# Optimization experiments

Hardware: AMD Instinct MI355X
Metric: run time of the kernel (lower is better)

## Reference

```python
import jax, jax.numpy as jnp
import numpy as np

DIMS = [128, 118, 109, 100, 92]  # dims[i+1] = max(int(dims[i]/1.081), 6)
NUM_SHELLS = 3
TARGET_COORD = 1.081
NUM_BASINS = 8
BATCH = 12288


def _pdist(a, b):
    # Euclidean pairwise distances [Na, Nb]
    a2 = jnp.sum(a * a, axis=-1)
    b2 = jnp.sum(b * b, axis=-1)
    d2 = a2[:, None] + b2[None, :] - 2.0 * (a @ b.T)
    return jnp.sqrt(jnp.clip(d2, 0.0, None))


def setup_inputs() -> dict:
    key = jax.random.key(0)
    ks = jax.random.split(key, 32)
    inp = {"x": jax.random.normal(ks[0], (BATCH, DIMS[0]), jnp.float32)}
    i = 1
    for s in range(4):
        din, dout = DIMS[s], DIMS[s + 1]
        sc = 1.0 / np.sqrt(din)
        inp[f"cw{s}"] = jax.random.uniform(ks[i], (dout, din), jnp.float32, -sc, sc); i += 1
        inp[f"cb{s}"] = jax.random.uniform(ks[i], (dout,), jnp.float32, -sc, sc); i += 1
        sc0 = 1.0 / np.sqrt(DIMS[0])
        inp[f"sw{s}"] = jax.random.uniform(ks[i], (dout, DIMS[0]), jnp.float32, -sc0, sc0); i += 1
        inp[f"sb{s}"] = jax.random.uniform(ks[i], (dout,), jnp.float32, -sc0, sc0); i += 1
    D = DIMS[-1]
    inp["shell_bnd"] = jnp.linspace(0.5, 2.0, NUM_SHELLS + 1, dtype=jnp.float32)
    scs = 1.0 / np.sqrt(NUM_SHELLS)
    inp["se_w"] = jax.random.uniform(ks[i], (D, NUM_SHELLS), jnp.float32, -scs, scs); i += 1
    inp["se_b"] = jax.random.uniform(ks[i], (D,), jnp.float32, -scs, scs); i += 1
    inp["basin_c"] = jax.random.normal(ks[i], (NUM_BASINS, D), jnp.float32) * 0.1; i += 1
    inp["basin_d"] = jnp.linspace(-6.48, -7.68, NUM_BASINS, dtype=jnp.float32)
    inp["basin_w"] = jnp.ones((NUM_BASINS,), jnp.float32) * 0.5
    return inp


def _forward(x, cws, cbs, sws, sbs, shell_bnd, se_w, se_b, basin_c, basin_d, basin_w):
    # CompressionTransform: Linear -> GELU (+ 0.1 * skip from input)
    cur = x
    for w, b, w2, b2 in zip(cws, cbs, sws, sbs):
        cur = jax.nn.gelu(cur @ w.T + b, approximate=False) + 0.1 * (x @ w2.T + b2)
    compressed = cur  # [B, 92]

    # EnergyLandscape: softmax basin mixture
    bdists = _pdist(compressed, basin_c)             # [B, num_basins]
    widths = jax.nn.softplus(basin_w)                # [num_basins]
    basin_probs = jax.nn.softmax(-bdists / widths, axis=-1)
    energy = jnp.sum(basin_probs * basin_d, axis=-1)  # [B]

    # CoordinationAnalysis: pairwise-distance shell histogram
    B = compressed.shape[0]
    dself = _pdist(compressed, compressed)           # [B, B]
    offdiag = ~jnp.eye(B, dtype=bool)
    bnd = jax.nn.softplus(shell_bnd)
    occ = jnp.stack(
        [jnp.sum(jnp.where(offdiag & (dself >= bnd[i]) & (dself < bnd[i + 1]), 1.0, 0.0), axis=-1)
         for i in range(NUM_SHELLS)],
        axis=-1,
    )  # [B, num_shells]
    occ = occ / (TARGET_COORD * (B - 1) + 1e-08)
    feats = compressed + occ @ se_w.T + se_b          # features with coordination info
    return feats, energy, basin_probs, occ


def reference(x, cw0, cb0, sw0, sb0, cw1, cb1, sw1, sb1, cw2, cb2, sw2, sb2,
              cw3, cb3, sw3, sb3, shell_bnd, se_w, se_b, basin_c, basin_d, basin_w):
    cws = [cw0, cw1, cw2, cw3]
    cbs = [cb0, cb1, cb2, cb3]
    sws = [sw0, sw1, sw2, sw3]
    sbs = [sb0, sb1, sb2, sb3]
    return _forward(x, cws, cbs, sws, sbs, shell_bnd, se_w, se_b, basin_c, basin_d, basin_w)
```

## Files before the change

kernel.cpp:

```cpp
#include <hip/hip_runtime.h>
#include <hip/hip_bf16.h>

typedef __attribute__((ext_vector_type(8))) short bf16x8;
typedef __attribute__((ext_vector_type(4))) float f32x4;
typedef unsigned short u16;

#define BATCH 12288

__device__ __forceinline__ u16 f2bf(float f){
  __hip_bfloat16 h = __float2bfloat16(f);
  return *reinterpret_cast<u16*>(&h);
}
__device__ __forceinline__ float bf2f(u16 u){
  __hip_bfloat16 h; *reinterpret_cast<u16*>(&h) = u;
  return __bfloat162float(h);
}
__device__ __forceinline__ f32x4 mfma16(bf16x8 a, bf16x8 b, f32x4 c){
  return __builtin_amdgcn_mfma_f32_16x16x32_bf16(a, b, c, 0, 0, 0);
}
__device__ __forceinline__ float softplusf(float v){ return log1pf(expf(v)); }

__global__ __launch_bounds__(256) void k_wconv8(
    const float* __restrict__ s0, const float* __restrict__ s1,
    const float* __restrict__ s2, const float* __restrict__ s3,
    const float* __restrict__ s4, const float* __restrict__ s5,
    const float* __restrict__ s6, const float* __restrict__ s7,
    u16* __restrict__ dst)
{
  int blk = blockIdx.x;
  int slab = blk >> 6;
  const float* src; int rows, cols;
  switch (slab){
    case 0: src = s0; rows = 118; cols = 128; break;
    case 1: src = s1; rows = 118; cols = 128; break;
    case 2: src = s2; rows = 109; cols = 118; break;
    case 3: src = s3; rows = 109; cols = 128; break;
    case 4: src = s4; rows = 100; cols = 109; break;
    case 5: src = s5; rows = 100; cols = 128; break;
    case 6: src = s6; rows =  92; cols = 100; break;
    default: src = s7; rows =  92; cols = 128; break;
  }
  int idx = (blk & 63) * 256 + threadIdx.x;
  int r = idx >> 7, c = idx & 127;
  float v = (r < rows && c < cols) ? src[r * cols + c] : 0.f;
  dst[slab * 16384 + idx] = f2bf(v);
}

__global__ __launch_bounds__(256) void k_mlp(const float* __restrict__ x,
    const u16* __restrict__ slabs,
    const float* __restrict__ cb0, const float* __restrict__ cb1,
    const float* __restrict__ cb2, const float* __restrict__ cb3,
    const float* __restrict__ sb0, const float* __restrict__ sb1,
    const float* __restrict__ sb2, const float* __restrict__ sb3,
    float* __restrict__ comp)
{
  const int LSTR = 136;
  __shared__ u16 xbf[32 * 136];
  __shared__ u16 act[2][32 * 136];
  int tid = threadIdx.x;
  int lane = tid & 63, w = tid >> 6;
  int fr = lane & 15, fg = lane >> 4;
  int r0 = blockIdx.x * 32;

  #pragma unroll
  for (int i = 0; i < 4; i++){
    int slot = tid + i * 256;
    int row = slot >> 5, c4 = slot & 31;
    float4 v = *reinterpret_cast<const float4*>(&x[(r0 + row) * 128 + c4 * 4]);
    ushort4 pk;
    pk.x = f2bf(v.x); pk.y = f2bf(v.y); pk.z = f2bf(v.z); pk.w = f2bf(v.w);
    *reinterpret_cast<ushort4*>(&xbf[row * LSTR + c4 * 4]) = pk;
  }
  __syncthreads();

  bf16x8 xa[2][4];
  #pragma unroll
  for (int mf = 0; mf < 2; mf++)
    #pragma unroll
    for (int kc = 0; kc < 4; kc++)
      xa[mf][kc] = *reinterpret_cast<const bf16x8*>(&xbf[(16*mf + fr) * LSTR + kc*32 + fg*8]);

  const float* cbs[4] = {cb0, cb1, cb2, cb3};
  const float* sbs[4] = {sb0, sb1, sb2, sb3};
  const int douts[4] = {118, 109, 100, 92};

  #pragma unroll
  for (int s = 0; s < 4; s++){
    const u16* aIn  = (s == 0) ? xbf : &act[(s + 1) & 1][0];
    u16*       aOut = &act[s & 1][0];
    const u16* cwS = slabs + (2*s)     * 16384;
    const u16* swS = slabs + (2*s + 1) * 16384;
    const float* cb = cbs[s];
    const float* sb = sbs[s];
    int dout = douts[s];

    bf16x8 af[2][4];
    #pragma unroll
    for (int mf = 0; mf < 2; mf++)
      #pragma unroll
      for (int kc = 0; kc < 4; kc++)
        af[mf][kc] = *reinterpret_cast<const bf16x8*>(&aIn[(16*mf + fr) * LSTR + kc*32 + fg*8]);

    f32x4 ac1[2][2], ac2[2][2];
    #pragma unroll
    for (int mf = 0; mf < 2; mf++)
      #pragma unroll
      for (int nf = 0; nf < 2; nf++){
        ac1[mf][nf] = (f32x4){0.f,0.f,0.f,0.f};
        ac2[mf][nf] = (f32x4){0.f,0.f,0.f,0.f};
      }

    #pragma unroll
    for (int nf = 0; nf < 2; nf++){
      int o = 32*w + 16*nf + fr;
      #pragma unroll
      for (int kc = 0; kc < 4; kc++){
        bf16x8 b1 = *reinterpret_cast<const bf16x8*>(&cwS[o * 128 + kc*32 + fg*8]);
        bf16x8 b2 = *reinterpret_cast<const bf16x8*>(&swS[o * 128 + kc*32 + fg*8]);
        ac1[0][nf] = mfma16(af[0][kc], b1, ac1[0][nf]);
        ac1[1][nf] = mfma16(af[1][kc], b1, ac1[1][nf]);
        ac2[0][nf] = mfma16(xa[0][kc], b2, ac2[0][nf]);
        ac2[1][nf] = mfma16(xa[1][kc], b2, ac2[1][nf]);
      }
    }

    #pragma unroll
    for (int nf = 0; nf < 2; nf++){
      int col = 32*w + 16*nf + fr;
      float cbv = (col < dout) ? cb[col] : 0.f;
      float sbv = (col < dout) ? sb[col] : 0.f;
      #pragma unroll
      for (int mf = 0; mf < 2; mf++){
        #pragma unroll
        for (int r = 0; r < 4; r++){
          float t1 = ac1[mf][nf][r] + cbv;
          float g = 0.5f * t1 * (1.f + erff(t1 * 0.70710678118654752f));
          float v = g + 0.1f * (ac2[mf][nf][r] + sbv);
          int row = 16*mf + fg*4 + r;
          if (s < 3){
            aOut[row * LSTR + col] = (col < dout) ? f2bf(v) : (u16)0;
          } else {
            if (col < 92) comp[(r0 + row) * 92 + col] = v;
          }
        }
      }
    }
    __syncthreads();
  }
}

__global__ __launch_bounds__(256) void k_rowfin(const float* __restrict__ comp,
    u16* __restrict__ Cbf, float* __restrict__ nrm2,
    const float* __restrict__ basin_c, const float* __restrict__ basin_d,
    const float* __restrict__ basin_w,
    float* __restrict__ energy_out, float* __restrict__ probs_out)
{
  int tid = threadIdx.x; int lane = tid & 63; int w = tid >> 6;
  int row = blockIdx.x * 4 + w;

  float c0 = comp[row * 92 + lane];
  int d2i = 64 + lane;
  float c1 = (d2i < 92) ? comp[row * 92 + d2i] : 0.f;

  u16 b0 = f2bf(c0);
  u16 b1 = (d2i < 92) ? f2bf(c1) : (u16)0;
  Cbf[row * 96 + lane] = b0;
  if (lane < 32) Cbf[row * 96 + 64 + lane] = b1;

  float f0 = bf2f(b0), f1 = bf2f(b1);
  float ns = f0*f0 + f1*f1;
  #pragma unroll
  for (int m = 1; m < 64; m <<= 1) ns += __shfl_xor(ns, m);
  if (lane == 0) nrm2[row] = -0.5f * ns;

  float bd[8];
  #pragma unroll
  for (int b = 0; b < 8; b++){
    float e0 = c0 - basin_c[b * 92 + lane];
    float p = e0 * e0;
    if (d2i < 92){ float e1 = c1 - basin_c[b * 92 + d2i]; p += e1 * e1; }
    #pragma unroll
    for (int m = 1; m < 64; m <<= 1) p += __shfl_xor(p, m);
    bd[b] = sqrtf(p);
  }
  float z[8]; float mx = -1e30f;
  #pragma unroll
  for (int b = 0; b < 8; b++){
    float wd = softplusf(basin_w[b]);
    z[b] = -bd[b] / wd;
    mx = fmaxf(mx, z[b]);
  }
  float p8[8]; float ssum = 0.f;
  #pragma unroll
  for (int b = 0; b < 8; b++){ p8[b] = expf(z[b] - mx); ssum += p8[b]; }
  float inv = 1.f / ssum; float en = 0.f;
  #pragma unroll
  for (int b = 0; b < 8; b++){ p8[b] *= inv; en += p8[b] * basin_d[b]; }

  if (lane == 0) energy_out[row] = en;
  if (lane < 8){
    float v = (lane & 4) ? ((lane & 2) ? ((lane & 1) ? p8[7] : p8[6])
                                       : ((lane & 1) ? p8[5] : p8[4]))
                         : ((lane & 2) ? ((lane & 1) ? p8[3] : p8[2])
                                       : ((lane & 1) ? p8[1] : p8[0]));
    probs_out[row * 8 + lane] = v;
  }
}

__global__ __launch_bounds__(256, 4) void k_pdist(const u16* __restrict__ Cbf,
    const float* __restrict__ nrm2, const float* __restrict__ shell_bnd,
    unsigned* __restrict__ cnt)
{
  __shared__ u16 Bs[2][64 * 104];
  __shared__ float Ns[2][64];
  int tid = threadIdx.x; int lane = tid & 63; int w = tid >> 6;
  int fr = lane & 15, fg = lane >> 4;
  int blk = blockIdx.x;
  int ib = blk % 96, jc = blk / 96;
  int i0 = ib * 128, j0 = jc * 384;

  float q0 = softplusf(shell_bnd[0]); float mq0 = -0.5f * q0 * q0;
  float q1 = softplusf(shell_bnd[1]); float mq1 = -0.5f * q1 * q1;
  float q2 = softplusf(shell_bnd[2]); float mq2 = -0.5f * q2 * q2;
  float q3 = softplusf(shell_bnd[3]); float mq3 = -0.5f * q3 * q3;

  int wrow0 = i0 + 32 * w;
  bf16x8 A[2][3];
  #pragma unroll
  for (int mf = 0; mf < 2; mf++)
    #pragma unroll
    for (int kc = 0; kc < 3; kc++)
      A[mf][kc] = *reinterpret_cast<const bf16x8*>(&Cbf[(wrow0 + 16*mf + fr) * 96 + kc*32 + fg*8]);

  float hr[2][4];
  #pragma unroll
  for (int mf = 0; mf < 2; mf++)
    #pragma unroll
    for (int r = 0; r < 4; r++)
      hr[mf][r] = nrm2[wrow0 + 16*mf + fg*4 + r];

  unsigned c[2][4][4];
  #pragma unroll
  for (int mf = 0; mf < 2; mf++)
    #pragma unroll
    for (int r = 0; r < 4; r++)
      #pragma unroll
      for (int t = 0; t < 4; t++) c[mf][r][t] = 0u;

  int srcR[3], srcS[3], dstL[3];
  #pragma unroll
  for (int t = 0; t < 3; t++){
    int ch = tid + t * 256;
    int rr = ch / 12, sl = ch - rr * 12;
    srcR[t] = rr; srcS[t] = sl * 8;
    dstL[t] = rr * 104 + sl * 8;
  }

  {
    int jr0 = j0;
    #pragma unroll
    for (int t = 0; t < 3; t++)
      *reinterpret_cast<bf16x8*>(&Bs[0][dstL[t]]) =
        *reinterpret_cast<const bf16x8*>(&Cbf[(jr0 + srcR[t]) * 96 + srcS[t]]);
    if (tid < 64) Ns[0][tid] = nrm2[jr0 + tid];
  }
  __syncthreads();

  for (int s = 0; s < 6; s++){
    int p = s & 1;
    if (s < 5){
      int jr0 = j0 + (s + 1) * 64;
      #pragma unroll
      for (int t = 0; t < 3; t++)
        *reinterpret_cast<bf16x8*>(&Bs[p ^ 1][dstL[t]]) =
          *reinterpret_cast<const bf16x8*>(&Cbf[(jr0 + srcR[t]) * 96 + srcS[t]]);
      if (tid < 64) Ns[p ^ 1][tid] = nrm2[jr0 + tid];
    }

    #pragma unroll
    for (int nt = 0; nt < 4; nt++){
      bf16x8 B0 = *reinterpret_cast<const bf16x8*>(&Bs[p][(nt*16 + fr) * 104 + 0*32 + fg*8]);
      bf16x8 B1 = *reinterpret_cast<const bf16x8*>(&Bs[p][(nt*16 + fr) * 104 + 1*32 + fg*8]);
      bf16x8 B2 = *reinterpret_cast<const bf16x8*>(&Bs[p][(nt*16 + fr) * 104 + 2*32 + fg*8]);
      float hc = Ns[p][nt*16 + fr];

      f32x4 g0, g1;
      #pragma unroll
      for (int r = 0; r < 4; r++){ g0[r] = hr[0][r] + hc; g1[r] = hr[1][r] + hc; }
      g0 = mfma16(A[0][0], B0, g0); g0 = mfma16(A[0][1], B1, g0); g0 = mfma16(A[0][2], B2, g0);
      g1 = mfma16(A[1][0], B0, g1); g1 = mfma16(A[1][1], B1, g1); g1 = mfma16(A[1][2], B2, g1);

      #pragma unroll
      for (int r = 0; r < 4; r++){
        float v0 = g0[r], v1 = g1[r];
        c[0][r][0] += (v0 <= mq0);
        c[0][r][1] += (v0 <= mq1);
        c[0][r][2] += (v0 <= mq2);
        c[0][r][3] += (v0 <= mq3);
        c[1][r][0] += (v1 <= mq0);
        c[1][r][1] += (v1 <= mq1);
        c[1][r][2] += (v1 <= mq2);
        c[1][r][3] += (v1 <= mq3);
      }
    }
    __syncthreads();
  }

  #pragma unroll
  for (int mf = 0; mf < 2; mf++)
    #pragma unroll
    for (int r = 0; r < 4; r++)
      #pragma unroll
      for (int t = 0; t < 4; t++){
        int v = (int)c[mf][r][t];
        v += __shfl_xor(v, 1); v += __shfl_xor(v, 2);
        v += __shfl_xor(v, 4); v += __shfl_xor(v, 8);
        c[mf][r][t] = (unsigned)v;
      }
  if (fr == 0){
    #pragma unroll
    for (int mf = 0; mf < 2; mf++)
      #pragma unroll
      for (int r = 0; r < 4; r++){
        int row = wrow0 + 16*mf + fg*4 + r;
        #pragma unroll
        for (int s = 0; s < 3; s++){
          unsigned o = c[mf][r][s] - c[mf][r][s + 1];
          if (o) atomicAdd(&cnt[row * 3 + s], o);
        }
      }
  }
}

__global__ __launch_bounds__(256) void k_feats(const float* __restrict__ comp,
    const unsigned* __restrict__ cnt, const float* __restrict__ se_w,
    const float* __restrict__ se_b, float* __restrict__ feats_out,
    float* __restrict__ occ_out)
{
  int tid = threadIdx.x; int lane = tid & 63; int w = tid >> 6;
  int row = blockIdx.x * 4 + w;
  const float denom = 1.081f * 12287.0f + 1e-8f;

  float o0 = (float)cnt[row * 3 + 0] / denom;
  float o1 = (float)cnt[row * 3 + 1] / denom;
  float o2 = (float)cnt[row * 3 + 2] / denom;

  {
    int d = lane;
    float v = comp[row * 92 + d]
            + o0 * se_w[d * 3 + 0] + o1 * se_w[d * 3 + 1] + o2 * se_w[d * 3 + 2]
            + se_b[d];
    feats_out[row * 92 + d] = v;
  }
  int d2 = lane + 64;
  if (d2 < 92){
    float v = comp[row * 92 + d2]
            + o0 * se_w[d2 * 3 + 0] + o1 * se_w[d2 * 3 + 1] + o2 * se_w[d2 * 3 + 2]
            + se_b[d2];
    feats_out[row * 92 + d2] = v;
  }
  if (lane < 3){
    float ov = (lane == 0) ? o0 : ((lane == 1) ? o1 : o2);
    occ_out[row * 3 + lane] = ov;
  }
}

extern "C" void kernel_launch(void* const* d_in, const int* in_sizes, int n_in,
                              void* d_out, int out_size, void* d_ws, size_t ws_size,
                              hipStream_t stream) {
  (void)in_sizes; (void)n_in; (void)out_size; (void)ws_size;

  const float* x = (const float*)d_in[0];
  const float* cw[4] = {(const float*)d_in[1], (const float*)d_in[5], (const float*)d_in[9],  (const float*)d_in[13]};
  const float* cb[4] = {(const float*)d_in[2], (const float*)d_in[6], (const float*)d_in[10], (const float*)d_in[14]};
  const float* sw[4] = {(const float*)d_in[3], (const float*)d_in[7], (const float*)d_in[11], (const float*)d_in[15]};
  const float* sb[4] = {(const float*)d_in[4], (const float*)d_in[8], (const float*)d_in[12], (const float*)d_in[16]};
  const float* shell_bnd = (const float*)d_in[17];
  const float* se_w = (const float*)d_in[18];
  const float* se_b = (const float*)d_in[19];
  const float* basin_c = (const float*)d_in[20];
  const float* basin_d = (const float*)d_in[21];
  const float* basin_w = (const float*)d_in[22];

  char* ws = (char*)d_ws;
  float*    comp  = (float*)(ws);
  u16*      Cbf   = (u16*)  (ws + 4521984);
  float*    nrm2  = (float*)(ws + 6881280);
  unsigned* cnt   = (unsigned*)(ws + 6930432);
  u16*      slabs = (u16*)  (ws + 7077888);

  float* out = (float*)d_out;
  float* feats_out  = out;
  float* energy_out = out + 1130496;
  float* probs_out  = out + 1142784;
  float* occ_out    = out + 1241088;

  hipMemsetAsync(cnt, 0, 147456, stream);

  k_wconv8<<<512, 256, 0, stream>>>(cw[0], sw[0], cw[1], sw[1], cw[2], sw[2], cw[3], sw[3],
                                    slabs);

  k_mlp<<<384, 256, 0, stream>>>(x, slabs,
      cb[0], cb[1], cb[2], cb[3], sb[0], sb[1], sb[2], sb[3], comp);

  k_rowfin<<<3072, 256, 0, stream>>>(comp, Cbf, nrm2, basin_c, basin_d, basin_w,
                                     energy_out, probs_out);

  k_pdist<<<3072, 256, 0, stream>>>(Cbf, nrm2, shell_bnd, cnt);

  k_feats<<<3072, 256, 0, stream>>>(comp, cnt, se_w, se_b, feats_out, occ_out);
}
```

Baseline: 137.4 us.

## Switch pairwise-distance histogram to 32x32x16 MFMA with inline-asm compare-add counting

Rewrites the k_pdist inner tile to use 32x32x16 bf16 MFMA instead of 16x16x32, so each wave computes a 32x32 block per instruction chain with a new operand and register layout. The shell counting is replaced by inline assembly that does v_cmp plus v_addc into the counters, avoiding separate select and add instructions. The launch-bounds occupancy hint is removed because the 16x4 counters and 16-wide accumulators need more registers. This can lower occupancy and adds a fifth shuffle step in the reduction.

```diff
diff --git a/kernel.cpp b/kernel.cpp
--- a/kernel.cpp
+++ b/kernel.cpp
@@ -3,6 +3,7 @@
 
 typedef __attribute__((ext_vector_type(8))) short bf16x8;
 typedef __attribute__((ext_vector_type(4))) float f32x4;
+typedef __attribute__((ext_vector_type(16))) float f32x16;
 typedef unsigned short u16;
 
 #define BATCH 12288
@@ -18,7 +19,25 @@
 __device__ __forceinline__ f32x4 mfma16(bf16x8 a, bf16x8 b, f32x4 c){
   return __builtin_amdgcn_mfma_f32_16x16x32_bf16(a, b, c, 0, 0, 0);
 }
+__device__ __forceinline__ f32x16 mfma32(bf16x8 a, bf16x8 b, f32x16 c){
+  return __builtin_amdgcn_mfma_f32_32x32x16_bf16(a, b, c, 0, 0, 0);
+}
 __device__ __forceinline__ float softplusf(float v){ return log1pf(expf(v)); }
+
+__device__ __forceinline__ void hist4(float v, float t0, float t1, float t2, float t3,
+                                      unsigned &c0, unsigned &c1, unsigned &c2, unsigned &c3){
+  asm("v_cmp_ngt_f32 vcc, %4, %5\n\t"
+      "v_addc_co_u32 %0, vcc, 0, %0, vcc\n\t"
+      "v_cmp_ngt_f32 vcc, %4, %6\n\t"
+      "v_addc_co_u32 %1, vcc, 0, %1, vcc\n\t"
+      "v_cmp_ngt_f32 vcc, %4, %7\n\t"
+      "v_addc_co_u32 %2, vcc, 0, %2, vcc\n\t"
+      "v_cmp_ngt_f32 vcc, %4, %8\n\t"
+      "v_addc_co_u32 %3, vcc, 0, %3, vcc"
+      : "+v"(c0), "+v"(c1), "+v"(c2), "+v"(c3)
+      : "v"(v), "v"(t0), "v"(t1), "v"(t2), "v"(t3)
+      : "vcc");
+}
 
 __global__ __launch_bounds__(256) void k_wconv8(
     const float* __restrict__ s0, const float* __restrict__ s1,
@@ -207,14 +226,14 @@
   }
 }
 
-__global__ __launch_bounds__(256, 4) void k_pdist(const u16* __restrict__ Cbf,
+__global__ __launch_bounds__(256) void k_pdist(const u16* __restrict__ Cbf,
     const float* __restrict__ nrm2, const float* __restrict__ shell_bnd,
     unsigned* __restrict__ cnt)
 {
   __shared__ u16 Bs[2][64 * 104];
   __shared__ float Ns[2][64];
   int tid = threadIdx.x; int lane = tid & 63; int w = tid >> 6;
-  int fr = lane & 15, fg = lane >> 4;
+  int l5 = lane & 31, hi = lane >> 5;
   int blk = blockIdx.x;
   int ib = blk % 96, jc = blk / 96;
   int i0 = ib * 128, j0 = jc * 384;
@@ -225,27 +244,22 @@
   float q3 = softplusf(shell_bnd[3]); float mq3 = -0.5f * q3 * q3;
 
   int wrow0 = i0 + 32 * w;
-  bf16x8 A[2][3];
-  #pragma unroll
-  for (int mf = 0; mf < 2; mf++)
-    #pragma unroll
-    for (int kc = 0; kc < 3; kc++)
-      A[mf][kc] = *reinterpret_cast<const bf16x8*>(&Cbf[(wrow0 + 16*mf + fr) * 96 + kc*32 + fg*8]);
-
-  float hr[2][4];
-  #pragma unroll
-  for (int mf = 0; mf < 2; mf++)
-    #pragma unroll
-    for (int r = 0; r < 4; r++)
-      hr[mf][r] = nrm2[wrow0 + 16*mf + fg*4 + r];
-
-  unsigned c[2][4][4];
-  #pragma unroll
-  for (int mf = 0; mf < 2; mf++)
-    #pragma unroll
-    for (int r = 0; r < 4; r++)
-      #pragma unroll
-      for (int t = 0; t < 4; t++) c[mf][r][t] = 0u;
+
+  bf16x8 A[6];
+  #pragma unroll
+  for (int ks = 0; ks < 6; ks++)
+    A[ks] = *reinterpret_cast<const bf16x8*>(&Cbf[(wrow0 + l5) * 96 + ks * 16 + hi * 8]);
+
+  float hr[16];
+  #pragma unroll
+  for (int t = 0; t < 16; t++)
+    hr[t] = nrm2[wrow0 + (t & 3) + 8 * (t >> 2) + 4 * hi];
+
+  unsigned c[16][4];
+  #pragma unroll
+  for (int t = 0; t < 16; t++)
+    #pragma unroll
+    for (int q = 0; q < 4; q++) c[t][q] = 0u;
 
   int srcR[3], srcS[3], dstL[3];
   #pragma unroll
@@ -278,57 +292,52 @@
     }
 
     #pragma unroll
-    for (int nt = 0; nt < 4; nt++){
-      bf16x8 B0 = *reinterpret_cast<const bf16x8*>(&Bs[p][(nt*16 + fr) * 104 + 0*32 + fg*8]);
-      bf16x8 B1 = *reinterpret_cast<const bf16x8*>(&Bs[p][(nt*16 + fr) * 104 + 1*32 + fg*8]);
-      bf16x8 B2 = *reinterpret_cast<const bf16x8*>(&Bs[p][(nt*16 + fr) * 104 + 2*32 + fg*8]);
-      float hc = Ns[p][nt*16 + fr];
-
-      f32x4 g0, g1;
-      #pragma unroll
-      for (int r = 0; r < 4; r++){ g0[r] = hr[0][r] + hc; g1[r] = hr[1][r] + hc; }
-      g0 = mfma16(A[0][0], B0, g0); g0 = mfma16(A[0][1], B1, g0); g0 = mfma16(A[0][2], B2, g0);
-      g1 = mfma16(A[1][0], B0, g1); g1 = mfma16(A[1][1], B1, g1); g1 = mfma16(A[1][2], B2, g1);
-
-      #pragma unroll
-      for (int r = 0; r < 4; r++){
-        float v0 = g0[r], v1 = g1[r];
-        c[0][r][0] += (v0 <= mq0);
-        c[0][r][1] += (v0 <= mq1);
-        c[0][r][2] += (v0 <= mq2);
-        c[0][r][3] += (v0 <= mq3);
-        c[1][r][0] += (v1 <= mq0);
-        c[1][r][1] += (v1 <= mq1);
-        c[1][r][2] += (v1 <= mq2);
-        c[1][r][3] += (v1 <= mq3);
+    for (int jt = 0; jt < 2; jt++){
+      int brow = jt * 32 + l5;
+      bf16x8 B0 = *reinterpret_cast<const bf16x8*>(&Bs[p][brow * 104 + 0*16 + hi*8]);
+      bf16x8 B1 = *reinterpret_cast<const bf16x8*>(&Bs[p][brow * 104 + 1*16 + hi*8]);
+      bf16x8 B2 = *reinterpret_cast<const bf16x8*>(&Bs[p][brow * 104 + 2*16 + hi*8]);
+      bf16x8 B3 = *reinterpret_cast<const bf16x8*>(&Bs[p][brow * 104 + 3*16 + hi*8]);
+      bf16x8 B4 = *reinterpret_cast<const bf16x8*>(&Bs[p][brow * 104 + 4*16 + hi*8]);
+      bf16x8 B5 = *reinterpret_cast<const bf16x8*>(&Bs[p][brow * 104 + 5*16 + hi*8]);
+      float hc = Ns[p][brow];
+
+      f32x16 g;
+      #pragma unroll
+      for (int t = 0; t < 16; t++) g[t] = hr[t] + hc;
+      g = mfma32(A[0], B0, g);
+      g = mfma32(A[1], B1, g);
+      g = mfma32(A[2], B2, g);
+      g = mfma32(A[3], B3, g);
+      g = mfma32(A[4], B4, g);
+      g = mfma32(A[5], B5, g);
+
+      #pragma unroll
+      for (int t = 0; t < 16; t++)
+        hist4(g[t], mq0, mq1, mq2, mq3, c[t][0], c[t][1], c[t][2], c[t][3]);
+    }
+    __syncthreads();
+  }
+
+  #pragma unroll
+  for (int t = 0; t < 16; t++)
+    #pragma unroll
+    for (int q = 0; q < 4; q++){
+      int v = (int)c[t][q];
+      v += __shfl_xor(v, 1); v += __shfl_xor(v, 2); v += __shfl_xor(v, 4);
+      v += __shfl_xor(v, 8); v += __shfl_xor(v, 16);
+      c[t][q] = (unsigned)v;
+    }
+  if (l5 == 0){
+    #pragma unroll
+    for (int t = 0; t < 16; t++){
+      int row = wrow0 + (t & 3) + 8 * (t >> 2) + 4 * hi;
+      #pragma unroll
+      for (int q = 0; q < 3; q++){
+        unsigned o = c[t][q] - c[t][q + 1];
+        if (o) atomicAdd(&cnt[row * 3 + q], o);
       }
     }
-    __syncthreads();
-  }
-
-  #pragma unroll
-  for (int mf = 0; mf < 2; mf++)
-    #pragma unroll
-    for (int r = 0; r < 4; r++)
-      #pragma unroll
-      for (int t = 0; t < 4; t++){
-        int v = (int)c[mf][r][t];
-        v += __shfl_xor(v, 1); v += __shfl_xor(v, 2);
-        v += __shfl_xor(v, 4); v += __shfl_xor(v, 8);
-        c[mf][r][t] = (unsigned)v;
-      }
-  if (fr == 0){
-    #pragma unroll
-    for (int mf = 0; mf < 2; mf++)
-      #pragma unroll
-      for (int r = 0; r < 4; r++){
-        int row = wrow0 + 16*mf + fg*4 + r;
-        #pragma unroll
-        for (int s = 0; s < 3; s++){
-          unsigned o = c[mf][r][s] - c[mf][r][s + 1];
-          if (o) atomicAdd(&cnt[row * 3 + s], o);
-        }
-      }
   }
 }
 
```

New measurement: 176.4 us. 28.4% more time.

## Exploit distance symmetry by computing only upper-triangular tile pairs in pdist

Applied to the files above, without the earlier changes.

The pairwise shell-count kernel now launches only upper-triangular 128x128 tile pairs (96*97/2 blocks), using a folded index mapping to balance work, and credits each distance to both the row and the column. Column counts are reduced across lane groups with shuffles and added atomically per tile, and diagonal tiles mask out the lower triangle and the self-pair. This roughly halves the MFMA and compare work, but adds many more atomics per block and removes the double-buffered B loading, so each block now does one load followed by compute with no overlap.

```diff
diff --git a/kernel.cpp b/kernel.cpp
--- a/kernel.cpp
+++ b/kernel.cpp
@@ -211,13 +211,18 @@
     const float* __restrict__ nrm2, const float* __restrict__ shell_bnd,
     unsigned* __restrict__ cnt)
 {
-  __shared__ u16 Bs[2][64 * 104];
-  __shared__ float Ns[2][64];
+  __shared__ u16 Bs[128 * 104];
+  __shared__ float Ns[128];
   int tid = threadIdx.x; int lane = tid & 63; int w = tid >> 6;
   int fr = lane & 15, fg = lane >> 4;
-  int blk = blockIdx.x;
-  int ib = blk % 96, jc = blk / 96;
-  int i0 = ib * 128, j0 = jc * 384;
+
+  int bid = blockIdx.x;
+  int a = bid / 97, b = bid - a * 97;
+  int ib, jb;
+  if (b < 96 - a){ ib = a;      jb = a + b; }
+  else           { ib = 95 - a; jb = 95 - a + (b - (96 - a)); }
+  int i0 = ib * 128, j0 = jb * 128;
+  bool diag = (ib == jb);
 
   float q0 = softplusf(shell_bnd[0]); float mq0 = -0.5f * q0 * q0;
   float q1 = softplusf(shell_bnd[1]); float mq1 = -0.5f * q1 * q1;
@@ -247,63 +252,58 @@
       #pragma unroll
       for (int t = 0; t < 4; t++) c[mf][r][t] = 0u;
 
-  int srcR[3], srcS[3], dstL[3];
-  #pragma unroll
-  for (int t = 0; t < 3; t++){
+  #pragma unroll
+  for (int t = 0; t < 6; t++){
     int ch = tid + t * 256;
     int rr = ch / 12, sl = ch - rr * 12;
-    srcR[t] = rr; srcS[t] = sl * 8;
-    dstL[t] = rr * 104 + sl * 8;
-  }
-
-  {
-    int jr0 = j0;
-    #pragma unroll
-    for (int t = 0; t < 3; t++)
-      *reinterpret_cast<bf16x8*>(&Bs[0][dstL[t]]) =
-        *reinterpret_cast<const bf16x8*>(&Cbf[(jr0 + srcR[t]) * 96 + srcS[t]]);
-    if (tid < 64) Ns[0][tid] = nrm2[jr0 + tid];
-  }
+    *reinterpret_cast<bf16x8*>(&Bs[rr * 104 + sl * 8]) =
+      *reinterpret_cast<const bf16x8*>(&Cbf[(j0 + rr) * 96 + sl * 8]);
+  }
+  if (tid < 128) Ns[tid] = nrm2[j0 + tid];
   __syncthreads();
 
-  for (int s = 0; s < 6; s++){
-    int p = s & 1;
-    if (s < 5){
-      int jr0 = j0 + (s + 1) * 64;
-      #pragma unroll
-      for (int t = 0; t < 3; t++)
-        *reinterpret_cast<bf16x8*>(&Bs[p ^ 1][dstL[t]]) =
-          *reinterpret_cast<const bf16x8*>(&Cbf[(jr0 + srcR[t]) * 96 + srcS[t]]);
-      if (tid < 64) Ns[p ^ 1][tid] = nrm2[jr0 + tid];
+  #pragma unroll
+  for (int nt = 0; nt < 8; nt++){
+    bf16x8 B0 = *reinterpret_cast<const bf16x8*>(&Bs[(nt*16 + fr) * 104 + 0*32 + fg*8]);
+    bf16x8 B1 = *reinterpret_cast<const bf16x8*>(&Bs[(nt*16 + fr) * 104 + 1*32 + fg*8]);
+    bf16x8 B2 = *reinterpret_cast<const bf16x8*>(&Bs[(nt*16 + fr) * 104 + 2*32 + fg*8]);
+    float hc = Ns[nt*16 + fr];
+    int jcol = j0 + nt*16 + fr;
+
+    f32x4 g0, g1;
+    #pragma unroll
+    for (int r = 0; r < 4; r++){ g0[r] = hr[0][r] + hc; g1[r] = hr[1][r] + hc; }
+    g0 = mfma16(A[0][0], B0, g0); g0 = mfma16(A[0][1], B1, g0); g0 = mfma16(A[0][2], B2, g0);
+    g1 = mfma16(A[1][0], B0, g1); g1 = mfma16(A[1][1], B1, g1); g1 = mfma16(A[1][2], B2, g1);
+
+    unsigned cc0 = 0, cc1 = 0, cc2 = 0, cc3 = 0;
+    #pragma unroll
+    for (int mf = 0; mf < 2; mf++)
+      #pragma unroll
+      for (int r = 0; r < 4; r++){
+        float v = (mf == 0) ? g0[r] : g1[r];
+        if (diag){
+          int irow = wrow0 + 16*mf + fg*4 + r;
+          v = (irow < jcol) ? v : 1.0f;
+        }
+        unsigned h0 = (v <= mq0) ? 1u : 0u;
+        unsigned h1 = (v <= mq1) ? 1u : 0u;
+        unsigned h2 = (v <= mq2) ? 1u : 0u;
+        unsigned h3 = (v <= mq3) ? 1u : 0u;
+        c[mf][r][0] += h0; c[mf][r][1] += h1; c[mf][r][2] += h2; c[mf][r][3] += h3;
+        cc0 += h0; cc1 += h1; cc2 += h2; cc3 += h3;
+      }
+
+    cc0 += __shfl_xor(cc0, 16); cc0 += __shfl_xor(cc0, 32);
+    cc1 += __shfl_xor(cc1, 16); cc1 += __shfl_xor(cc1, 32);
+    cc2 += __shfl_xor(cc2, 16); cc2 += __shfl_xor(cc2, 32);
+    cc3 += __shfl_xor(cc3, 16); cc3 += __shfl_xor(cc3, 32);
+    if (fg == 0){
+      unsigned o0 = cc0 - cc1, o1 = cc1 - cc2, o2 = cc2 - cc3;
+      if (o0) atomicAdd(&cnt[jcol * 3 + 0], o0);
+      if (o1) atomicAdd(&cnt[jcol * 3 + 1], o1);
+      if (o2) atomicAdd(&cnt[jcol * 3 + 2], o2);
     }
-
-    #pragma unroll
-    for (int nt = 0; nt < 4; nt++){
-      bf16x8 B0 = *reinterpret_cast<const bf16x8*>(&Bs[p][(nt*16 + fr) * 104 + 0*32 + fg*8]);
-      bf16x8 B1 = *reinterpret_cast<const bf16x8*>(&Bs[p][(nt*16 + fr) * 104 + 1*32 + fg*8]);
-      bf16x8 B2 = *reinterpret_cast<const bf16x8*>(&Bs[p][(nt*16 + fr) * 104 + 2*32 + fg*8]);
-      float hc = Ns[p][nt*16 + fr];
-
-      f32x4 g0, g1;
-      #pragma unroll
-      for (int r = 0; r < 4; r++){ g0[r] = hr[0][r] + hc; g1[r] = hr[1][r] + hc; }
-      g0 = mfma16(A[0][0], B0, g0); g0 = mfma16(A[0][1], B1, g0); g0 = mfma16(A[0][2], B2, g0);
-      g1 = mfma16(A[1][0], B0, g1); g1 = mfma16(A[1][1], B1, g1); g1 = mfma16(A[1][2], B2, g1);
-
-      #pragma unroll
-      for (int r = 0; r < 4; r++){
-        float v0 = g0[r], v1 = g1[r];
-        c[0][r][0] += (v0 <= mq0);
-        c[0][r][1] += (v0 <= mq1);
-        c[0][r][2] += (v0 <= mq2);
-        c[0][r][3] += (v0 <= mq3);
-        c[1][r][0] += (v1 <= mq0);
-        c[1][r][1] += (v1 <= mq1);
-        c[1][r][2] += (v1 <= mq2);
-        c[1][r][3] += (v1 <= mq3);
-      }
-    }
-    __syncthreads();
   }
 
   #pragma unroll
@@ -324,9 +324,9 @@
       for (int r = 0; r < 4; r++){
         int row = wrow0 + 16*mf + fg*4 + r;
         #pragma unroll
-        for (int s = 0; s < 3; s++){
-          unsigned o = c[mf][r][s] - c[mf][r][s + 1];
-          if (o) atomicAdd(&cnt[row * 3 + s], o);
+        for (int t = 0; t < 3; t++){
+          unsigned o = c[mf][r][t] - c[mf][r][t + 1];
+          if (o) atomicAdd(&cnt[row * 3 + t], o);
         }
       }
   }
@@ -406,7 +406,7 @@
   k_rowfin<<<3072, 256, 0, stream>>>(comp, Cbf, nrm2, basin_c, basin_d, basin_w,
                                      energy_out, probs_out);
 
-  k_pdist<<<3072, 256, 0, stream>>>(Cbf, nrm2, shell_bnd, cnt);
+  k_pdist<<<4656, 256, 0, stream>>>(Cbf, nrm2, shell_bnd, cnt);
 
   k_feats<<<3072, 256, 0, stream>>>(comp, cnt, se_w, se_b, feats_out, occ_out);
 }
```

Result: slower. 376.8 us (+174.2%).
